# Performance work log

Hardware: AMD Instinct MI355X
Metric: run time of the kernel (lower is better)

Reference implementation:

```python
import jax, jax.numpy as jnp
import numpy as np

B, S, D, H, FF = 4, 2048, 1024, 16, 4096
HD = D // H


def setup_inputs() -> dict:
    key = jax.random.key(0)
    ks = jax.random.split(key, 12)
    s = 1.0 / np.sqrt(D)
    sf = 1.0 / np.sqrt(FF)
    return {
        "x": jax.random.normal(ks[0], (B, S, D), dtype=jnp.float32),
        "lengths": jax.random.randint(ks[1], (B,), 1, S + 1, dtype=jnp.int32),
        "qW": jax.random.uniform(ks[2], (D, D), jnp.float32, -s, s),
        "qb": jnp.zeros((D,), jnp.float32),
        "kW": jax.random.uniform(ks[3], (D, D), jnp.float32, -s, s),
        "kb": jnp.zeros((D,), jnp.float32),
        "vW": jax.random.uniform(ks[4], (D, D), jnp.float32, -s, s),
        "vb": jnp.zeros((D,), jnp.float32),
        "oW": jax.random.uniform(ks[5], (D, D), jnp.float32, -s, s),
        "ob": jnp.zeros((D,), jnp.float32),
        "w1": jax.random.uniform(ks[6], (D, FF), jnp.float32, -s, s),
        "b1": jnp.zeros((FF,), jnp.float32),
        "w2": jax.random.uniform(ks[7], (FF, D), jnp.float32, -sf, sf),
        "b2": jnp.zeros((D,), jnp.float32),
    }


def _heads(t):
    # [B,S,D] -> [B,H,S,HD]
    return t.reshape(B, S, H, HD).transpose(0, 2, 1, 3)


def reference(x, lengths, qW, qb, kW, kb, vW, vb, oW, ob, w1, b1, w2, b2):
    q = _heads(x @ qW + qb)
    k = _heads(x @ kW + kb)
    v = _heads(x @ vW + vb)
    scale = 1.0 / np.sqrt(HD)
    logits = jnp.einsum("bhqd,bhkd->bhqk", q, k) * scale  # [B,H,S,S]
    # key-position mask: pos >= length -> -inf
    mask = jnp.arange(S)[None, None, None, :] >= lengths[:, None, None, None]
    logits = jnp.where(mask, -jnp.inf, logits)
    a = jax.nn.softmax(logits, axis=-1)
    ctx = jnp.einsum("bhqk,bhkd->bhqd", a, v)
    ctx = ctx.transpose(0, 2, 1, 3).reshape(B, S, D)
    attn_out = ctx @ oW + ob
    h = jax.nn.relu(attn_out @ w1 + b1)
    return h @ w2 + b2
```

## Files before the change

kernel.cpp:

```cpp
#include <hip/hip_runtime.h>


typedef short bf16x8 __attribute__((ext_vector_type(8)));
typedef float f32x4 __attribute__((ext_vector_type(4)));

__device__ __forceinline__ unsigned short f2bf(float f) {
  unsigned int u = __builtin_bit_cast(unsigned int, f);
  u += 0x7fffu + ((u >> 16) & 1u);
  return (unsigned short)(u >> 16);
}

__device__ __forceinline__ void gload16(const unsigned short* g, unsigned short* l) {
  __builtin_amdgcn_global_load_lds(
      (const __attribute__((address_space(1))) unsigned int*)(g),
      (__attribute__((address_space(3))) unsigned int*)(l),
      16, 0, 0);
}

__global__ __launch_bounds__(256) void cast_f32_bf16(
    const float* __restrict__ src, unsigned short* __restrict__ dst, int n4) {
  int i = blockIdx.x * 256 + threadIdx.x;
  if (i < n4) {
    float4 f = ((const float4*)src)[i];
    ushort4 o;
    o.x = f2bf(f.x); o.y = f2bf(f.y); o.z = f2bf(f.z); o.w = f2bf(f.w);
    ((ushort4*)dst)[i] = o;
  }
}

__global__ __launch_bounds__(256) void prep_weights(
    const float* __restrict__ qW, const float* __restrict__ kW,
    const float* __restrict__ vW, const float* __restrict__ oW,
    const float* __restrict__ w1, const float* __restrict__ w2,
    unsigned short* __restrict__ qWt, unsigned short* __restrict__ kWt,
    unsigned short* __restrict__ vWt, unsigned short* __restrict__ oWt,
    unsigned short* __restrict__ w1t, unsigned short* __restrict__ w2t) {
  const int t = blockIdx.x;
  const float* W; unsigned short* Wt; int N, K, nt, kt;
  if (t < 2048) {
    const int w = t >> 9, r = t & 511;
    nt = r & 15; kt = r >> 4; N = 1024; K = 1024;
    W  = w == 0 ? qW : w == 1 ? kW : w == 2 ? vW : oW;
    Wt = w == 0 ? qWt : w == 1 ? kWt : w == 2 ? vWt : oWt;
  } else if (t < 4096) {
    const int r = t - 2048;
    nt = r & 63; kt = r >> 6; N = 4096; K = 1024; W = w1; Wt = w1t;
  } else {
    const int r = t - 4096;
    nt = r & 15; kt = r >> 4; N = 1024; K = 4096; W = w2; Wt = w2t;
  }
  const int wave = threadIdx.x >> 6, lane = threadIdx.x & 63;
  const int n = nt * 64 + lane;
  const int k0 = kt * 32 + wave * 8;
  union { int4 v; unsigned short u[8]; } s;
#pragma unroll
  for (int j = 0; j < 8; ++j) s.u[j] = f2bf(W[(size_t)(k0 + j) * N + n]);
  *(int4*)(Wt + (size_t)n * K + k0) = s.v;
}

__device__ __forceinline__ void gemm256_core(
    const unsigned short* __restrict__ A, const unsigned short* __restrict__ Bt,
    unsigned short* __restrict__ As, unsigned short* __restrict__ Bs,
    const int m0, const int n0, const int K, f32x4 (&acc)[8][4]) {
  const int tid = (int)threadIdx.x;
  const int w = tid >> 6, l = tid & 63;
  const int quad = l >> 4, l16 = l & 15;
  const int wm = (w >> 2) * 128, wn = (w & 3) * 64;

  const int lr = l >> 2, lc = l & 3;
  const int swz = (lc ^ ((l >> 3) & 3)) * 8;
  const unsigned short* gA[2]; const unsigned short* gB[2];
  unsigned short* dA[2]; unsigned short* dB[2];
#pragma unroll
  for (int j = 0; j < 2; ++j) {
    const int rr = (w * 2 + j) * 16 + lr;
    gA[j] = A + (size_t)(m0 + rr) * K + swz;
    gB[j] = Bt + (size_t)(n0 + rr) * K + swz;
    dA[j] = As + (w * 2 + j) * 512;
    dB[j] = Bs + (w * 2 + j) * 512;
  }

  const int cread = (quad ^ ((l16 >> 1) & 3)) * 8;
  const int rA = (wm + l16) * 32;
  const int rB = (wn + l16) * 32;

  auto STAGE = [&](int db, int t) {
#pragma unroll
    for (int j = 0; j < 2; ++j) {
      gload16(gA[j] + t * 32, dA[j] + db * 8192);
      gload16(gB[j] + t * 32, dB[j] + db * 8192);
    }
  };
  auto COMPUTE = [&](int db) {
    bf16x8 af[8], bf[4];
    const unsigned short* pa = As + db * 8192 + rA + cread;
    const unsigned short* pb = Bs + db * 8192 + rB + cread;
#pragma unroll
    for (int ni = 0; ni < 4; ++ni) bf[ni] = *(const bf16x8*)(pb + ni * 16 * 32);
#pragma unroll
    for (int mi = 0; mi < 8; ++mi) af[mi] = *(const bf16x8*)(pa + mi * 16 * 32);
    __builtin_amdgcn_s_setprio(1);
#pragma unroll
    for (int mi = 0; mi < 8; ++mi)
#pragma unroll
      for (int ni = 0; ni < 4; ++ni)
        acc[mi][ni] = __builtin_amdgcn_mfma_f32_16x16x32_bf16(
            af[mi], bf[ni], acc[mi][ni], 0, 0, 0);
    __builtin_amdgcn_s_setprio(0);
  };

  const int NK = K >> 5;
  STAGE(0, 0); STAGE(1, 1); STAGE(2, 2);
#pragma unroll 1
  for (int t = 0; t < NK - 3; ++t) {
    asm volatile("s_waitcnt vmcnt(8)" ::: "memory");
    __builtin_amdgcn_s_barrier();
    STAGE((t + 3) & 3, t + 3);
    COMPUTE(t & 3);
  }
  asm volatile("s_waitcnt vmcnt(8)" ::: "memory");
  __builtin_amdgcn_s_barrier();
  COMPUTE((NK - 3) & 3);
  asm volatile("s_waitcnt vmcnt(4)" ::: "memory");
  __builtin_amdgcn_s_barrier();
  COMPUTE((NK - 2) & 3);
  asm volatile("s_waitcnt vmcnt(0)" ::: "memory");
  __builtin_amdgcn_s_barrier();
  COMPUTE((NK - 1) & 3);
}

__device__ __forceinline__ void gemm128_core(
    const unsigned short* __restrict__ A, const unsigned short* __restrict__ Bt,
    unsigned short* __restrict__ As, unsigned short* __restrict__ Bs,
    const int m0, const int n0, const int K, f32x4 (&acc)[4][4]) {
  const int tid = (int)threadIdx.x;
  const int w = tid >> 6, l = tid & 63;
  const int quad = l >> 4, l16 = l & 15;
  const int wm = (w >> 1) * 64, wn = (w & 1) * 64;

  const int lr = l >> 2, lc = l & 3;
  const int swz = (lc ^ ((l >> 3) & 3)) * 8;
  const unsigned short* gA[2]; const unsigned short* gB[2];
  unsigned short* dA[2]; unsigned short* dB[2];
#pragma unroll
  for (int j = 0; j < 2; ++j) {
    const int rr = (w * 2 + j) * 16 + lr;
    gA[j] = A + (size_t)(m0 + rr) * K + swz;
    gB[j] = Bt + (size_t)(n0 + rr) * K + swz;
    dA[j] = As + (w * 2 + j) * 512;
    dB[j] = Bs + (w * 2 + j) * 512;
  }

  const int cread = (quad ^ ((l16 >> 1) & 3)) * 8;
  const int rA = (wm + l16) * 32;
  const int rB = (wn + l16) * 32;

  auto STAGE = [&](int db, int t) {
#pragma unroll
    for (int j = 0; j < 2; ++j) {
      gload16(gA[j] + t * 32, dA[j] + db * 4096);
      gload16(gB[j] + t * 32, dB[j] + db * 4096);
    }
  };
  auto COMPUTE = [&](int db) {
    bf16x8 af[4], bf[4];
    const unsigned short* pa = As + db * 4096 + rA + cread;
    const unsigned short* pb = Bs + db * 4096 + rB + cread;
#pragma unroll
    for (int ni = 0; ni < 4; ++ni) bf[ni] = *(const bf16x8*)(pb + ni * 16 * 32);
#pragma unroll
    for (int mi = 0; mi < 4; ++mi) af[mi] = *(const bf16x8*)(pa + mi * 16 * 32);
    __builtin_amdgcn_s_setprio(1);
#pragma unroll
    for (int mi = 0; mi < 4; ++mi)
#pragma unroll
      for (int ni = 0; ni < 4; ++ni)
        acc[mi][ni] = __builtin_amdgcn_mfma_f32_16x16x32_bf16(
            af[mi], bf[ni], acc[mi][ni], 0, 0, 0);
    __builtin_amdgcn_s_setprio(0);
  };

  const int NK = K >> 5;
  STAGE(0, 0); STAGE(1, 1); STAGE(2, 2);
#pragma unroll 1
  for (int t = 0; t < NK - 3; ++t) {
    asm volatile("s_waitcnt vmcnt(8)" ::: "memory");
    __builtin_amdgcn_s_barrier();
    STAGE((t + 3) & 3, t + 3);
    COMPUTE(t & 3);
  }
  asm volatile("s_waitcnt vmcnt(8)" ::: "memory");
  __builtin_amdgcn_s_barrier();
  COMPUTE((NK - 3) & 3);
  asm volatile("s_waitcnt vmcnt(4)" ::: "memory");
  __builtin_amdgcn_s_barrier();
  COMPUTE((NK - 2) & 3);
  asm volatile("s_waitcnt vmcnt(0)" ::: "memory");
  __builtin_amdgcn_s_barrier();
  COMPUTE((NK - 1) & 3);
}

template <int EPI>
__global__ __launch_bounds__(512, 1) void gemm256_bt(
    const unsigned short* __restrict__ A, const unsigned short* __restrict__ Bt,
    const float* __restrict__ bias, void* __restrict__ C, int N, int K) {
  __shared__ unsigned short As[4 * 8192];
  __shared__ unsigned short Bs[4 * 8192];
  const int tn = N >> 8;
  const int cpx = (int)gridDim.x >> 3;
  const int sw = ((int)blockIdx.x & 7) * cpx + ((int)blockIdx.x >> 3);
  const int nt = sw % tn, mt = sw / tn;
  const int m0 = mt * 256, n0 = nt * 256;

  f32x4 acc[8][4] = {};
  gemm256_core(A, Bt, As, Bs, m0, n0, K, acc);

  const int tid = (int)threadIdx.x;
  const int w = tid >> 6, l = tid & 63;
  const int quad = l >> 4, l16 = l & 15;
  const int wm = (w >> 2) * 128, wn = (w & 3) * 64;
#pragma unroll
  for (int ni = 0; ni < 4; ++ni) {
    const int col = n0 + wn + ni * 16 + l16;
    const float bv = bias[col];
#pragma unroll
    for (int mi = 0; mi < 8; ++mi) {
      const int row = m0 + wm + mi * 16 + quad * 4;
#pragma unroll
      for (int r = 0; r < 4; ++r) {
        float v = acc[mi][ni][r] + bv;
        if (EPI == 2) v = v > 0.f ? v : 0.f;
        if (EPI == 0)
          ((float*)C)[(size_t)(row + r) * N + col] = v;
        else
          ((unsigned short*)C)[(size_t)(row + r) * N + col] = f2bf(v);
      }
    }
  }
}

template <int EPI>
__global__ __launch_bounds__(256, 2) void gemm128_bt(
    const unsigned short* __restrict__ A, const unsigned short* __restrict__ Bt,
    const float* __restrict__ bias, void* __restrict__ C, int N, int K) {
  __shared__ unsigned short As[4 * 4096];
  __shared__ unsigned short Bs[4 * 4096];
  const int NT = N >> 7, band = NT >> 3;
  const int xcd = blockIdx.x & 7, local = blockIdx.x >> 3;
  const int nt = xcd * band + local % band;
  const int mt = local / band;
  const int m0 = mt * 128, n0 = nt * 128;

  f32x4 acc[4][4] = {};
  gemm128_core(A, Bt, As, Bs, m0, n0, K, acc);

  const int tid = (int)threadIdx.x;
  const int w = tid >> 6, l = tid & 63;
  const int quad = l >> 4, l16 = l & 15;
  const int wm = (w >> 1) * 64, wn = (w & 1) * 64;
#pragma unroll
  for (int ni = 0; ni < 4; ++ni) {
    const int col = n0 + wn + ni * 16 + l16;
    const float bv = bias[col];
#pragma unroll
    for (int mi = 0; mi < 4; ++mi) {
      const int row = m0 + wm + mi * 16 + quad * 4;
#pragma unroll
      for (int r = 0; r < 4; ++r) {
        float v = acc[mi][ni][r] + bv;
        if (EPI == 2) v = v > 0.f ? v : 0.f;
        if (EPI == 0)
          ((float*)C)[(size_t)(row + r) * N + col] = v;
        else
          ((unsigned short*)C)[(size_t)(row + r) * N + col] = f2bf(v);
      }
    }
  }
}

#define QSCALE 0.180336884f

__global__ __launch_bounds__(256, 2) void gemm128_qkv(
    const unsigned short* __restrict__ A, const unsigned short* __restrict__ Bt,
    const float* __restrict__ qb, const float* __restrict__ kb,
    const float* __restrict__ vb, unsigned short* __restrict__ Qo,
    unsigned short* __restrict__ Ko, unsigned short* __restrict__ Vto, int K) {
  __shared__ unsigned short As[4 * 4096];
  __shared__ unsigned short Bs[4 * 4096];
  const int NT = 24, band = 3;
  const int xcd = blockIdx.x & 7, local = blockIdx.x >> 3;
  const int nt = xcd * band + local % band;
  const int mt = local / band;
  const int m0 = mt * 128, n0 = nt * 128;

  f32x4 acc[4][4] = {};
  gemm128_core(A, Bt, As, Bs, m0, n0, K, acc);

  const int tid = (int)threadIdx.x;
  const int w = tid >> 6, l = tid & 63;
  const int quad = l >> 4, l16 = l & 15;
  const int wm = (w >> 1) * 64, wn = (w & 1) * 64;

  const int seg = n0 >> 10;
  const float* bias = seg == 0 ? qb : (seg == 1 ? kb : vb);
#pragma unroll
  for (int ni = 0; ni < 4; ++ni) {
    const int col = (n0 + wn + ni * 16 + l16) & 1023;
    const float bv = bias[col];
#pragma unroll
    for (int mi = 0; mi < 4; ++mi) {
      const int row = m0 + wm + mi * 16 + quad * 4;
      if (seg == 2) {
        const int b = row >> 11, s = row & 2047;
        const int hh = col >> 6, dh = col & 63;
        union { ushort4 v; unsigned short u[4]; } pk;
#pragma unroll
        for (int r = 0; r < 4; ++r) pk.u[r] = f2bf(acc[mi][ni][r] + bv);
        *(ushort4*)(Vto + ((size_t)((b * 16 + hh) * 64 + dh)) * 2048 + s) = pk.v;
      } else if (seg == 0) {
#pragma unroll
        for (int r = 0; r < 4; ++r)
          Qo[(size_t)(row + r) * 1024 + col] = f2bf((acc[mi][ni][r] + bv) * QSCALE);
      } else {
#pragma unroll
        for (int r = 0; r < 4; ++r)
          Ko[(size_t)(row + r) * 1024 + col] = f2bf(acc[mi][ni][r] + bv);
      }
    }
  }
}

__global__ __launch_bounds__(256, 4) void attn_fused(
    const unsigned short* __restrict__ Q, const unsigned short* __restrict__ K,
    const unsigned short* __restrict__ Vt, const int* __restrict__ lengths,
    unsigned short* __restrict__ ctx) {
  constexpr int S = 2048, D = 1024;
  __shared__ unsigned short Ks[64 * 72];
  __shared__ unsigned short Vs[64 * 72];
  __shared__ unsigned short Ps[4 * 32 * 72];

  const int tid = threadIdx.x;
  const int wave = tid >> 6, lane = tid & 63;
  const int quad = lane >> 4, l16 = lane & 15;
  const int bid = blockIdx.x;
  const int qt = bid & 15;
  const int h = (bid >> 4) & 15;
  const int b = bid >> 8;
  const int q0 = qt * 128;
  const int len = lengths[b];
  const int ktEnd = (len + 63) >> 6;
  const float NEGINF = -__builtin_inff();

  const size_t xbase = (size_t)b * S * D + (size_t)h * 64;
  const size_t vtb = (size_t)(b * 16 + h) * 64;

  bf16x8 qf0[2], qf1[2];
#pragma unroll
  for (int mb = 0; mb < 2; ++mb) {
    const unsigned short* qrow =
        Q + xbase + (size_t)(q0 + wave * 32 + mb * 16 + l16) * D;
    qf0[mb] = *(const bf16x8*)(qrow + quad * 8);
    qf1[mb] = *(const bf16x8*)(qrow + 32 + quad * 8);
  }

  const int sr1 = tid >> 3, sc1 = (tid & 7) * 8;
  const int sr2 = (256 + tid) >> 3, sc2 = (tid & 7) * 8;
  const unsigned short* kg1 = K + xbase + (size_t)sr1 * D + sc1;
  const unsigned short* kg2 = K + xbase + (size_t)sr2 * D + sc2;
  const unsigned short* vg1 = Vt + (vtb + sr1) * S + sc1;
  const unsigned short* vg2 = Vt + (vtb + sr2) * S + sc2;

  f32x4 oacc[2][4] = {};
  float rs[2][4] = {};

  unsigned short* pw = Ps + wave * (32 * 72);

  int4 kr1, kr2, vr1, vr2;
  {
    kr1 = *(const int4*)(kg1);
    kr2 = *(const int4*)(kg2);
    vr1 = *(const int4*)(vg1);
    vr2 = *(const int4*)(vg2);
  }

  for (int kt = 0; kt < ktEnd; ++kt) {
    const int k0 = kt * 64;
    __syncthreads();
    *(int4*)(Ks + sr1 * 72 + sc1) = kr1;
    *(int4*)(Ks + sr2 * 72 + sc2) = kr2;
    *(int4*)(Vs + sr1 * 72 + sc1) = vr1;
    *(int4*)(Vs + sr2 * 72 + sc2) = vr2;
    __syncthreads();

    if (kt + 1 < ktEnd) {
      const int kn = (kt + 1) * 64;
      kr1 = *(const int4*)(kg1 + (size_t)kn * D);
      kr2 = *(const int4*)(kg2 + (size_t)kn * D);
      vr1 = *(const int4*)(vg1 + kn);
      vr2 = *(const int4*)(vg2 + kn);
    }

    f32x4 sf[2][4];
#pragma unroll
    for (int cb = 0; cb < 4; ++cb) {
      const bf16x8 kf0 = *(const bf16x8*)(Ks + (cb * 16 + l16) * 72 + quad * 8);
      const bf16x8 kf1 = *(const bf16x8*)(Ks + (cb * 16 + l16) * 72 + 32 + quad * 8);
#pragma unroll
      for (int mb = 0; mb < 2; ++mb) {
        f32x4 c = {0.f, 0.f, 0.f, 0.f};
        c = __builtin_amdgcn_mfma_f32_16x16x32_bf16(qf0[mb], kf0, c, 0, 0, 0);
        c = __builtin_amdgcn_mfma_f32_16x16x32_bf16(qf1[mb], kf1, c, 0, 0, 0);
        sf[mb][cb] = c;
      }
    }

    if (k0 + 64 > len) {
#pragma unroll
      for (int cb = 0; cb < 4; ++cb) {
        const bool msk = (k0 + cb * 16 + l16) >= len;
#pragma unroll
        for (int mb = 0; mb < 2; ++mb)
#pragma unroll
          for (int r = 0; r < 4; ++r) sf[mb][cb][r] = msk ? NEGINF : sf[mb][cb][r];
      }
    }

#pragma unroll
    for (int mb = 0; mb < 2; ++mb)
#pragma unroll
      for (int cb = 0; cb < 4; ++cb)
#pragma unroll
        for (int r = 0; r < 4; ++r) {
          const float p = __builtin_amdgcn_exp2f(sf[mb][cb][r]);
          sf[mb][cb][r] = p;
          rs[mb][r] += p;
        }

#pragma unroll
    for (int mb = 0; mb < 2; ++mb)
#pragma unroll
      for (int cb = 0; cb < 4; ++cb)
#pragma unroll
        for (int r = 0; r < 4; ++r)
          pw[(mb * 16 + quad * 4 + r) * 72 + cb * 16 + l16] = f2bf(sf[mb][cb][r]);

    bf16x8 pa0[2], pa1[2];
#pragma unroll
    for (int mb = 0; mb < 2; ++mb) {
      pa0[mb] = *(const bf16x8*)(pw + (mb * 16 + l16) * 72 + quad * 8);
      pa1[mb] = *(const bf16x8*)(pw + (mb * 16 + l16) * 72 + 32 + quad * 8);
    }
#pragma unroll
    for (int cb = 0; cb < 4; ++cb) {
      const bf16x8 vb0 = *(const bf16x8*)(Vs + (cb * 16 + l16) * 72 + quad * 8);
      const bf16x8 vb1 = *(const bf16x8*)(Vs + (cb * 16 + l16) * 72 + 32 + quad * 8);
#pragma unroll
      for (int mb = 0; mb < 2; ++mb) {
        oacc[mb][cb] = __builtin_amdgcn_mfma_f32_16x16x32_bf16(pa0[mb], vb0, oacc[mb][cb], 0, 0, 0);
        oacc[mb][cb] = __builtin_amdgcn_mfma_f32_16x16x32_bf16(pa1[mb], vb1, oacc[mb][cb], 0, 0, 0);
      }
    }
  }

#pragma unroll
  for (int off = 8; off > 0; off >>= 1)
#pragma unroll
    for (int mb = 0; mb < 2; ++mb)
#pragma unroll
      for (int r = 0; r < 4; ++r) rs[mb][r] += __shfl_xor(rs[mb][r], off, 16);

#pragma unroll
  for (int mb = 0; mb < 2; ++mb) {
    float inv[4];
#pragma unroll
    for (int r = 0; r < 4; ++r) inv[r] = 1.0f / rs[mb][r];
#pragma unroll
    for (int cb = 0; cb < 4; ++cb)
#pragma unroll
      for (int r = 0; r < 4; ++r) {
        const int row = q0 + wave * 32 + mb * 16 + quad * 4 + r;
        ctx[xbase + (size_t)row * D + cb * 16 + l16] = f2bf(oacc[mb][cb][r] * inv[r]);
      }
  }
}

extern "C" void kernel_launch(void* const* d_in, const int* in_sizes, int n_in,
                              void* d_out, int out_size, void* d_ws,
                              size_t ws_size, hipStream_t stream) {
  const float* x  = (const float*)d_in[0];
  const int* lengths = (const int*)d_in[1];
  const float* qW = (const float*)d_in[2];
  const float* qb = (const float*)d_in[3];
  const float* kW = (const float*)d_in[4];
  const float* kb = (const float*)d_in[5];
  const float* vW = (const float*)d_in[6];
  const float* vb = (const float*)d_in[7];
  const float* oW = (const float*)d_in[8];
  const float* ob = (const float*)d_in[9];
  const float* w1 = (const float*)d_in[10];
  const float* b1 = (const float*)d_in[11];
  const float* w2 = (const float*)d_in[12];
  const float* b2 = (const float*)d_in[13];
  float* out = (float*)d_out;

  const int Bx = 4, S = 2048, D = 1024, FF = 4096;
  const int M = Bx * S;

  unsigned short* p = (unsigned short*)d_ws;
  unsigned short* xb  = p; p += (size_t)M * D;
  unsigned short* qWt = p; p += (size_t)D * D;
  unsigned short* kWt = p; p += (size_t)D * D;
  unsigned short* vWt = p; p += (size_t)D * D;
  unsigned short* oWt = p; p += (size_t)D * D;
  unsigned short* w1t = p; p += (size_t)D * FF;
  unsigned short* w2t = p; p += (size_t)FF * D;
  unsigned short* Qb  = p; p += (size_t)M * D;
  unsigned short* Kb  = p; p += (size_t)M * D;
  unsigned short* Vtb = p; p += (size_t)M * D;
  unsigned short* Cb  = p; p += (size_t)M * D;
  unsigned short* Ab  = p; p += (size_t)M * D;
  unsigned short* Hb  = p; p += (size_t)M * FF;

  {
    int n4 = (int)((size_t)M * D / 4);
    cast_f32_bf16<<<dim3((n4 + 255) / 256), dim3(256), 0, stream>>>(x, xb, n4);
  }
  prep_weights<<<dim3(6144), dim3(256), 0, stream>>>(
      qW, kW, vW, oW, w1, w2, qWt, kWt, vWt, oWt, w1t, w2t);

  gemm128_qkv<<<dim3(1536), dim3(256), 0, stream>>>(
      xb, qWt, qb, kb, vb, Qb, Kb, Vtb, D);

  attn_fused<<<dim3(Bx * 16 * (S / 128)), dim3(256), 0, stream>>>(
      Qb, Kb, Vtb, lengths, Cb);

  gemm128_bt<1><<<dim3(512), dim3(256), 0, stream>>>(Cb, oWt, ob, Ab, D, D);
  gemm256_bt<2><<<dim3(512), dim3(512), 0, stream>>>(Ab, w1t, b1, Hb, FF, D);
  gemm128_bt<0><<<dim3(512), dim3(256), 0, stream>>>(Hb, w2t, b2, out, D, FF);
}
```

Baseline: 505.2 us.

## Use 8-phase interleaved 256x256 GEMM core with K=64 tiles for QKV and FFN1

Replaces the four-stage, K=32 256-tile GEMM core with a double-buffered K=64 core. It splits each K step into four quadrant MFMA phases, with global-to-LDS loads and LDS reads interleaved between barriers and a new XOR swizzle. The QKV projection moves from 128x128 tiles with 1536 blocks to this 256x256 kernel with 384 blocks, which raises reuse per tile. In exchange it adds many more barriers, runs fewer blocks per CU, and may leave the QKV grid unevenly spread across CUs.

```diff
diff --git a/kernel.cpp b/kernel.cpp
--- a/kernel.cpp
+++ b/kernel.cpp
@@ -58,7 +58,7 @@
   *(int4*)(Wt + (size_t)n * K + k0) = s.v;
 }
 
-__device__ __forceinline__ void gemm256_core(
+__device__ __forceinline__ void gemm256_8ph(
     const unsigned short* __restrict__ A, const unsigned short* __restrict__ Bt,
     unsigned short* __restrict__ As, unsigned short* __restrict__ Bs,
     const int m0, const int n0, const int K, f32x4 (&acc)[8][4]) {
@@ -67,6 +67,196 @@
   const int quad = l >> 4, l16 = l & 15;
   const int wm = (w >> 2) * 128, wn = (w & 3) * 64;
 
+  const int srow = w * 8 + (l >> 3);
+  const int schunk = ((l & 7) ^ (l >> 3)) * 8;
+  const unsigned short* gA = A + (size_t)(m0 + srow) * K + schunk;
+  const unsigned short* gB = Bt + (size_t)(n0 + srow) * K + schunk;
+  const int ldsW = w * 512;
+
+  const int xr = l16 & 7;
+  const int c0 = ((0 + quad) ^ xr) * 8;
+  const int c1 = ((4 + quad) ^ xr) * 8;
+
+  bf16x8 af[4][2], bf0[2][2], bf1[2][2];
+
+  auto STA = [&](int buf, int a, int t) {
+    gload16(gA + (size_t)(a * 64) * K + t * 64,
+            As + buf * 16384 + a * 4096 + ldsW);
+  };
+  auto STB = [&](int buf, int a, int t) {
+    gload16(gB + (size_t)(a * 64) * K + t * 64,
+            Bs + buf * 16384 + a * 4096 + ldsW);
+  };
+  auto LDA = [&](int buf, int mh) {
+    const unsigned short* p = As + buf * 16384 + (wm + mh * 64 + l16) * 64;
+#pragma unroll
+    for (int mi = 0; mi < 4; ++mi) {
+      af[mi][0] = *(const bf16x8*)(p + mi * 16 * 64 + c0);
+      af[mi][1] = *(const bf16x8*)(p + mi * 16 * 64 + c1);
+    }
+  };
+  auto LDB = [&](int buf, int nh, bf16x8 (&bf)[2][2]) {
+    const unsigned short* p = Bs + buf * 16384 + (wn + nh * 32 + l16) * 64;
+#pragma unroll
+    for (int ni = 0; ni < 2; ++ni) {
+      bf[ni][0] = *(const bf16x8*)(p + ni * 16 * 64 + c0);
+      bf[ni][1] = *(const bf16x8*)(p + ni * 16 * 64 + c1);
+    }
+  };
+  auto MM = [&](int mh, int nh, bf16x8 (&bf)[2][2]) {
+    __builtin_amdgcn_s_setprio(1);
+#pragma unroll
+    for (int mi = 0; mi < 4; ++mi)
+#pragma unroll
+      for (int ni = 0; ni < 2; ++ni) {
+        f32x4& a = acc[mh * 4 + mi][nh * 2 + ni];
+        a = __builtin_amdgcn_mfma_f32_16x16x32_bf16(af[mi][0], bf[ni][0], a, 0, 0, 0);
+        a = __builtin_amdgcn_mfma_f32_16x16x32_bf16(af[mi][1], bf[ni][1], a, 0, 0, 0);
+      }
+    __builtin_amdgcn_s_setprio(0);
+  };
+
+  const int NK = K >> 6;
+  STB(0, 0, 0); STB(0, 1, 0); STB(0, 2, 0); STB(0, 3, 0);
+  STA(0, 0, 0); STA(0, 2, 0); STA(0, 1, 0); STA(0, 3, 0);
+  asm volatile("s_waitcnt vmcnt(2)" ::: "memory");
+  __builtin_amdgcn_s_barrier();
+
+#pragma unroll 1
+  for (int t = 0; t < NK; ++t) {
+    const int c = t & 1, nb = c ^ 1;
+    const bool st = (t + 1 < NK);
+    LDA(c, 0); LDB(c, 0, bf0);
+    if (st) { STB(nb, 0, t + 1); STB(nb, 1, t + 1); }
+    __builtin_amdgcn_s_barrier();
+    asm volatile("s_waitcnt lgkmcnt(0)" ::: "memory");
+    __builtin_amdgcn_sched_barrier(0);
+    MM(0, 0, bf0);
+    __builtin_amdgcn_s_barrier();
+    LDB(c, 1, bf1);
+    if (st) { STB(nb, 2, t + 1); STB(nb, 3, t + 1); }
+    __builtin_amdgcn_s_barrier();
+    asm volatile("s_waitcnt lgkmcnt(0)" ::: "memory");
+    __builtin_amdgcn_sched_barrier(0);
+    MM(0, 1, bf1);
+    if (st) asm volatile("s_waitcnt vmcnt(4)" ::: "memory");
+    else    asm volatile("s_waitcnt vmcnt(0)" ::: "memory");
+    __builtin_amdgcn_s_barrier();
+    LDA(c, 1);
+    if (st) { STA(nb, 0, t + 1); STA(nb, 2, t + 1); }
+    __builtin_amdgcn_s_barrier();
+    asm volatile("s_waitcnt lgkmcnt(0)" ::: "memory");
+    __builtin_amdgcn_sched_barrier(0);
+    MM(1, 1, bf1);
+    __builtin_amdgcn_s_barrier();
+    if (st) { STA(nb, 1, t + 1); STA(nb, 3, t + 1); }
+    __builtin_amdgcn_s_barrier();
+    MM(1, 0, bf0);
+    if (st) asm volatile("s_waitcnt vmcnt(2)" ::: "memory");
+    __builtin_amdgcn_s_barrier();
+  }
+}
+
+template <int EPI>
+__global__ __launch_bounds__(512, 1) void gemm256_bt(
+    const unsigned short* __restrict__ A, const unsigned short* __restrict__ Bt,
+    const float* __restrict__ bias, void* __restrict__ C, int N, int K) {
+  __shared__ unsigned short As[2 * 16384];
+  __shared__ unsigned short Bs[2 * 16384];
+  const int tn = N >> 8;
+  const int cpx = (int)gridDim.x >> 3;
+  const int sw = ((int)blockIdx.x & 7) * cpx + ((int)blockIdx.x >> 3);
+  const int nt = sw % tn, mt = sw / tn;
+  const int m0 = mt * 256, n0 = nt * 256;
+
+  f32x4 acc[8][4] = {};
+  gemm256_8ph(A, Bt, As, Bs, m0, n0, K, acc);
+
+  const int tid = (int)threadIdx.x;
+  const int w = tid >> 6, l = tid & 63;
+  const int quad = l >> 4, l16 = l & 15;
+  const int wm = (w >> 2) * 128, wn = (w & 3) * 64;
+#pragma unroll
+  for (int ni = 0; ni < 4; ++ni) {
+    const int col = n0 + wn + ni * 16 + l16;
+    const float bv = bias[col];
+#pragma unroll
+    for (int mi = 0; mi < 8; ++mi) {
+      const int row = m0 + wm + mi * 16 + quad * 4;
+#pragma unroll
+      for (int r = 0; r < 4; ++r) {
+        float v = acc[mi][ni][r] + bv;
+        if (EPI == 2) v = v > 0.f ? v : 0.f;
+        if (EPI == 0)
+          ((float*)C)[(size_t)(row + r) * N + col] = v;
+        else
+          ((unsigned short*)C)[(size_t)(row + r) * N + col] = f2bf(v);
+      }
+    }
+  }
+}
+
+#define QSCALE 0.180336884f
+
+__global__ __launch_bounds__(512, 1) void gemm256_qkv(
+    const unsigned short* __restrict__ A, const unsigned short* __restrict__ Bt,
+    const float* __restrict__ qb, const float* __restrict__ kb,
+    const float* __restrict__ vb, unsigned short* __restrict__ Qo,
+    unsigned short* __restrict__ Ko, unsigned short* __restrict__ Vto, int K) {
+  __shared__ unsigned short As[2 * 16384];
+  __shared__ unsigned short Bs[2 * 16384];
+  const int tn = 12;
+  const int cpx = (int)gridDim.x >> 3;
+  const int sw = ((int)blockIdx.x & 7) * cpx + ((int)blockIdx.x >> 3);
+  const int nt = sw % tn, mt = sw / tn;
+  const int m0 = mt * 256, n0 = nt * 256;
+
+  f32x4 acc[8][4] = {};
+  gemm256_8ph(A, Bt, As, Bs, m0, n0, K, acc);
+
+  const int tid = (int)threadIdx.x;
+  const int w = tid >> 6, l = tid & 63;
+  const int quad = l >> 4, l16 = l & 15;
+  const int wm = (w >> 2) * 128, wn = (w & 3) * 64;
+
+  const int seg = n0 >> 10;
+  const float* bias = seg == 0 ? qb : (seg == 1 ? kb : vb);
+#pragma unroll
+  for (int ni = 0; ni < 4; ++ni) {
+    const int col = (n0 + wn + ni * 16 + l16) & 1023;
+    const float bv = bias[col];
+#pragma unroll
+    for (int mi = 0; mi < 8; ++mi) {
+      const int row = m0 + wm + mi * 16 + quad * 4;
+      if (seg == 2) {
+        const int b = row >> 11, s = row & 2047;
+        const int hh = col >> 6, dh = col & 63;
+        union { ushort4 v; unsigned short u[4]; } pk;
+#pragma unroll
+        for (int r = 0; r < 4; ++r) pk.u[r] = f2bf(acc[mi][ni][r] + bv);
+        *(ushort4*)(Vto + ((size_t)((b * 16 + hh) * 64 + dh)) * 2048 + s) = pk.v;
+      } else if (seg == 0) {
+#pragma unroll
+        for (int r = 0; r < 4; ++r)
+          Qo[(size_t)(row + r) * 1024 + col] = f2bf((acc[mi][ni][r] + bv) * QSCALE);
+      } else {
+#pragma unroll
+        for (int r = 0; r < 4; ++r)
+          Ko[(size_t)(row + r) * 1024 + col] = f2bf(acc[mi][ni][r] + bv);
+      }
+    }
+  }
+}
+
+__device__ __forceinline__ void gemm128_core(
+    const unsigned short* __restrict__ A, const unsigned short* __restrict__ Bt,
+    unsigned short* __restrict__ As, unsigned short* __restrict__ Bs,
+    const int m0, const int n0, const int K, f32x4 (&acc)[4][4]) {
+  const int tid = (int)threadIdx.x;
+  const int w = tid >> 6, l = tid & 63;
+  const int quad = l >> 4, l16 = l & 15;
+  const int wm = (w >> 1) * 64, wn = (w & 1) * 64;
+
   const int lr = l >> 2, lc = l & 3;
   const int swz = (lc ^ ((l >> 3) & 3)) * 8;
   const unsigned short* gA[2]; const unsigned short* gB[2];
@@ -87,21 +277,21 @@
   auto STAGE = [&](int db, int t) {
 #pragma unroll
     for (int j = 0; j < 2; ++j) {
-      gload16(gA[j] + t * 32, dA[j] + db * 8192);
-      gload16(gB[j] + t * 32, dB[j] + db * 8192);
+      gload16(gA[j] + t * 32, dA[j] + db * 4096);
+      gload16(gB[j] + t * 32, dB[j] + db * 4096);
     }
   };
   auto COMPUTE = [&](int db) {
-    bf16x8 af[8], bf[4];
-    const unsigned short* pa = As + db * 8192 + rA + cread;
-    const unsigned short* pb = Bs + db * 8192 + rB + cread;
+    bf16x8 af[4], bf[4];
+    const unsigned short* pa = As + db * 4096 + rA + cread;
+    const unsigned short* pb = Bs + db * 4096 + rB + cread;
 #pragma unroll
     for (int ni = 0; ni < 4; ++ni) bf[ni] = *(const bf16x8*)(pb + ni * 16 * 32);
 #pragma unroll
-    for (int mi = 0; mi < 8; ++mi) af[mi] = *(const bf16x8*)(pa + mi * 16 * 32);
+    for (int mi = 0; mi < 4; ++mi) af[mi] = *(const bf16x8*)(pa + mi * 16 * 32);
     __builtin_amdgcn_s_setprio(1);
 #pragma unroll
-    for (int mi = 0; mi < 8; ++mi)
+    for (int mi = 0; mi < 4; ++mi)
 #pragma unroll
       for (int ni = 0; ni < 4; ++ni)
         acc[mi][ni] = __builtin_amdgcn_mfma_f32_16x16x32_bf16(
@@ -127,116 +317,6 @@
   asm volatile("s_waitcnt vmcnt(0)" ::: "memory");
   __builtin_amdgcn_s_barrier();
   COMPUTE((NK - 1) & 3);
-}
-
-__device__ __forceinline__ void gemm128_core(
-    const unsigned short* __restrict__ A, const unsigned short* __restrict__ Bt,
-    unsigned short* __restrict__ As, unsigned short* __restrict__ Bs,
-    const int m0, const int n0, const int K, f32x4 (&acc)[4][4]) {
-  const int tid = (int)threadIdx.x;
-  const int w = tid >> 6, l = tid & 63;
-  const int quad = l >> 4, l16 = l & 15;
-  const int wm = (w >> 1) * 64, wn = (w & 1) * 64;
-
-  const int lr = l >> 2, lc = l & 3;
-  const int swz = (lc ^ ((l >> 3) & 3)) * 8;
-  const unsigned short* gA[2]; const unsigned short* gB[2];
-  unsigned short* dA[2]; unsigned short* dB[2];
-#pragma unroll
-  for (int j = 0; j < 2; ++j) {
-    const int rr = (w * 2 + j) * 16 + lr;
-    gA[j] = A + (size_t)(m0 + rr) * K + swz;
-    gB[j] = Bt + (size_t)(n0 + rr) * K + swz;
-    dA[j] = As + (w * 2 + j) * 512;
-    dB[j] = Bs + (w * 2 + j) * 512;
-  }
-
-  const int cread = (quad ^ ((l16 >> 1) & 3)) * 8;
-  const int rA = (wm + l16) * 32;
-  const int rB = (wn + l16) * 32;
-
-  auto STAGE = [&](int db, int t) {
-#pragma unroll
-    for (int j = 0; j < 2; ++j) {
-      gload16(gA[j] + t * 32, dA[j] + db * 4096);
-      gload16(gB[j] + t * 32, dB[j] + db * 4096);
-    }
-  };
-  auto COMPUTE = [&](int db) {
-    bf16x8 af[4], bf[4];
-    const unsigned short* pa = As + db * 4096 + rA + cread;
-    const unsigned short* pb = Bs + db * 4096 + rB + cread;
-#pragma unroll
-    for (int ni = 0; ni < 4; ++ni) bf[ni] = *(const bf16x8*)(pb + ni * 16 * 32);
-#pragma unroll
-    for (int mi = 0; mi < 4; ++mi) af[mi] = *(const bf16x8*)(pa + mi * 16 * 32);
-    __builtin_amdgcn_s_setprio(1);
-#pragma unroll
-    for (int mi = 0; mi < 4; ++mi)
-#pragma unroll
-      for (int ni = 0; ni < 4; ++ni)
-        acc[mi][ni] = __builtin_amdgcn_mfma_f32_16x16x32_bf16(
-            af[mi], bf[ni], acc[mi][ni], 0, 0, 0);
-    __builtin_amdgcn_s_setprio(0);
-  };
-
-  const int NK = K >> 5;
-  STAGE(0, 0); STAGE(1, 1); STAGE(2, 2);
-#pragma unroll 1
-  for (int t = 0; t < NK - 3; ++t) {
-    asm volatile("s_waitcnt vmcnt(8)" ::: "memory");
-    __builtin_amdgcn_s_barrier();
-    STAGE((t + 3) & 3, t + 3);
-    COMPUTE(t & 3);
-  }
-  asm volatile("s_waitcnt vmcnt(8)" ::: "memory");
-  __builtin_amdgcn_s_barrier();
-  COMPUTE((NK - 3) & 3);
-  asm volatile("s_waitcnt vmcnt(4)" ::: "memory");
-  __builtin_amdgcn_s_barrier();
-  COMPUTE((NK - 2) & 3);
-  asm volatile("s_waitcnt vmcnt(0)" ::: "memory");
-  __builtin_amdgcn_s_barrier();
-  COMPUTE((NK - 1) & 3);
-}
-
-template <int EPI>
-__global__ __launch_bounds__(512, 1) void gemm256_bt(
-    const unsigned short* __restrict__ A, const unsigned short* __restrict__ Bt,
-    const float* __restrict__ bias, void* __restrict__ C, int N, int K) {
-  __shared__ unsigned short As[4 * 8192];
-  __shared__ unsigned short Bs[4 * 8192];
-  const int tn = N >> 8;
-  const int cpx = (int)gridDim.x >> 3;
-  const int sw = ((int)blockIdx.x & 7) * cpx + ((int)blockIdx.x >> 3);
-  const int nt = sw % tn, mt = sw / tn;
-  const int m0 = mt * 256, n0 = nt * 256;
-
-  f32x4 acc[8][4] = {};
-  gemm256_core(A, Bt, As, Bs, m0, n0, K, acc);
-
-  const int tid = (int)threadIdx.x;
-  const int w = tid >> 6, l = tid & 63;
-  const int quad = l >> 4, l16 = l & 15;
-  const int wm = (w >> 2) * 128, wn = (w & 3) * 64;
-#pragma unroll
-  for (int ni = 0; ni < 4; ++ni) {
-    const int col = n0 + wn + ni * 16 + l16;
-    const float bv = bias[col];
-#pragma unroll
-    for (int mi = 0; mi < 8; ++mi) {
-      const int row = m0 + wm + mi * 16 + quad * 4;
-#pragma unroll
-      for (int r = 0; r < 4; ++r) {
-        float v = acc[mi][ni][r] + bv;
-        if (EPI == 2) v = v > 0.f ? v : 0.f;
-        if (EPI == 0)
-          ((float*)C)[(size_t)(row + r) * N + col] = v;
-        else
-          ((unsigned short*)C)[(size_t)(row + r) * N + col] = f2bf(v);
-      }
-    }
-  }
 }
 
 template <int EPI>
@@ -273,58 +353,6 @@
           ((float*)C)[(size_t)(row + r) * N + col] = v;
         else
           ((unsigned short*)C)[(size_t)(row + r) * N + col] = f2bf(v);
-      }
-    }
-  }
-}
-
-#define QSCALE 0.180336884f
-
-__global__ __launch_bounds__(256, 2) void gemm128_qkv(
-    const unsigned short* __restrict__ A, const unsigned short* __restrict__ Bt,
-    const float* __restrict__ qb, const float* __restrict__ kb,
-    const float* __restrict__ vb, unsigned short* __restrict__ Qo,
-    unsigned short* __restrict__ Ko, unsigned short* __restrict__ Vto, int K) {
-  __shared__ unsigned short As[4 * 4096];
-  __shared__ unsigned short Bs[4 * 4096];
-  const int NT = 24, band = 3;
-  const int xcd = blockIdx.x & 7, local = blockIdx.x >> 3;
-  const int nt = xcd * band + local % band;
-  const int mt = local / band;
-  const int m0 = mt * 128, n0 = nt * 128;
-
-  f32x4 acc[4][4] = {};
-  gemm128_core(A, Bt, As, Bs, m0, n0, K, acc);
-
-  const int tid = (int)threadIdx.x;
-  const int w = tid >> 6, l = tid & 63;
-  const int quad = l >> 4, l16 = l & 15;
-  const int wm = (w >> 1) * 64, wn = (w & 1) * 64;
-
-  const int seg = n0 >> 10;
-  const float* bias = seg == 0 ? qb : (seg == 1 ? kb : vb);
-#pragma unroll
-  for (int ni = 0; ni < 4; ++ni) {
-    const int col = (n0 + wn + ni * 16 + l16) & 1023;
-    const float bv = bias[col];
-#pragma unroll
-    for (int mi = 0; mi < 4; ++mi) {
-      const int row = m0 + wm + mi * 16 + quad * 4;
-      if (seg == 2) {
-        const int b = row >> 11, s = row & 2047;
-        const int hh = col >> 6, dh = col & 63;
-        union { ushort4 v; unsigned short u[4]; } pk;
-#pragma unroll
-        for (int r = 0; r < 4; ++r) pk.u[r] = f2bf(acc[mi][ni][r] + bv);
-        *(ushort4*)(Vto + ((size_t)((b * 16 + hh) * 64 + dh)) * 2048 + s) = pk.v;
-      } else if (seg == 0) {
-#pragma unroll
-        for (int r = 0; r < 4; ++r)
-          Qo[(size_t)(row + r) * 1024 + col] = f2bf((acc[mi][ni][r] + bv) * QSCALE);
-      } else {
-#pragma unroll
-        for (int r = 0; r < 4; ++r)
-          Ko[(size_t)(row + r) * 1024 + col] = f2bf(acc[mi][ni][r] + bv);
       }
     }
   }
@@ -528,7 +556,7 @@
   prep_weights<<<dim3(6144), dim3(256), 0, stream>>>(
       qW, kW, vW, oW, w1, w2, qWt, kWt, vWt, oWt, w1t, w2t);
 
-  gemm128_qkv<<<dim3(1536), dim3(256), 0, stream>>>(
+  gemm256_qkv<<<dim3(384), dim3(512), 0, stream>>>(
       xb, qWt, qb, kb, vb, Qb, Kb, Vtb, D);
 
   attn_fused<<<dim3(Bx * 16 * (S / 128)), dim3(256), 0, stream>>>(
```

Result: faster. 490.6 us (-2.9%).
